# Kernel optimization log

Measured on AMD Instinct MI355X. Metric: run time of the kernel, lower is better.

The kernel has to match this reference:

```python
import jax, jax.numpy as jnp
import numpy as np

HEADS = 16
HEAD_DIM = 64
EMBED = HEADS * HEAD_DIM  # 1024
B, S = 2, 2048


def setup_inputs() -> dict:
    key = jax.random.key(0)
    ks = jax.random.split(key, 9)
    return {
        "value": jax.random.normal(ks[0], (B, S, EMBED), dtype=jnp.float32),
        "key": jax.random.normal(ks[1], (B, S, EMBED), dtype=jnp.float32),
        "query": jax.random.normal(ks[2], (B, S, EMBED), dtype=jnp.float32),
        "mask": jax.random.randint(ks[3], (B, 1, S, S), 0, 2, dtype=jnp.int32),
        "Wq": jax.random.normal(ks[4], (HEAD_DIM, HEAD_DIM), dtype=jnp.float32) * 0.02,
        "Wk": jax.random.normal(ks[5], (HEAD_DIM, HEAD_DIM), dtype=jnp.float32) * 0.02,
        "Wv": jax.random.normal(ks[6], (HEAD_DIM, HEAD_DIM), dtype=jnp.float32) * 0.02,
        "Wo": jax.random.normal(ks[7], (EMBED, EMBED), dtype=jnp.float32) * 0.02,
        "bo": jnp.zeros((EMBED,), dtype=jnp.float32),
    }


def reference(value, key, query, mask, Wq, Wk, Wv, Wo, bo):
    N, Lv = value.shape[0], value.shape[1]
    Lk, Lq = key.shape[1], query.shape[1]
    # Faithful to original: plain reshape (N, heads, len, head_dim), NOT transpose.
    v = value.reshape(N, HEADS, Lv, HEAD_DIM)
    k = key.reshape(N, HEADS, Lk, HEAD_DIM)
    q = query.reshape(N, HEADS, Lq, HEAD_DIM)
    # Per-head Linear (no bias): x @ W.T
    V = jnp.einsum('bhld,ed->bhle', v, Wv)
    K = jnp.einsum('bhld,ed->bhle', k, Wk)
    Q = jnp.einsum('bhld,ed->bhle', q, Wq)
    score = jnp.einsum('bhqd,bhkd->bhqk', Q, K)  # [B,H,Sq,Sk]
    score = jnp.where(mask == 0, jnp.float32(-1e20), score)
    # Faithful quirk: scale by sqrt(embed_size), not sqrt(head_dim)
    scale = jnp.float32(EMBED ** 0.5)
    attn = jax.nn.softmax(score / scale, axis=3)
    out = jnp.einsum('bhqk,bhkd->bhqd', attn, V).reshape(N, Lq, HEADS * HEAD_DIM)
    return out @ Wo.T + bo
```

## Files before the change

### kernel.cpp

```cpp
#include <hip/hip_runtime.h>
#include <hip/hip_bf16.h>
#include <cstdint>
#include <cstddef>

#define S_LEN 2048
#define N_HEADS 16
#define HD 64
#define EMB 1024
#define N_BATCH 2
#define N_BH (N_BATCH * N_HEADS)

typedef __attribute__((ext_vector_type(4))) float f32x4;
typedef __attribute__((ext_vector_type(16))) float f32x16;
typedef __attribute__((ext_vector_type(8))) short short8;
typedef __attribute__((ext_vector_type(8))) _Float16 half8;

__device__ __forceinline__ f32x4 mfma16h(half8 a, half8 b, f32x4 c) {
    return __builtin_amdgcn_mfma_f32_16x16x32_f16(a, b, c, 0, 0, 0);
}
__device__ __forceinline__ f32x16 mfma32h(half8 a, half8 b, f32x16 c) {
    return __builtin_amdgcn_mfma_f32_32x32x16_f16(a, b, c, 0, 0, 0);
}

__device__ __forceinline__ unsigned pkh(float a, float b) {
    return __builtin_bit_cast(unsigned, __builtin_amdgcn_cvt_pkrtz(a, b));
}

#if __has_builtin(__builtin_amdgcn_exp2f)
__device__ __forceinline__ float fast_exp2(float x) { return __builtin_amdgcn_exp2f(x); }
#else
__device__ __forceinline__ float fast_exp2(float x) { return exp2f(x); }
#endif

__global__ __launch_bounds__(256) void prep_kernel(
    const float* __restrict__ q_in, const float* __restrict__ k_in,
    const float* __restrict__ v_in,
    const float* __restrict__ Wq, const float* __restrict__ Wk,
    const float* __restrict__ Wv, const float* __restrict__ Wo,
    const int* __restrict__ mask,
    short* __restrict__ Qb, short* __restrict__ Kb, short* __restrict__ Vt,
    short* __restrict__ Woh, unsigned long long* __restrict__ bits) {
    __shared__ short Al[64 * 72];
    __shared__ short Wl[64 * 72];
    __shared__ short Ol[64 * 72];
    int bx = blockIdx.x;
    int t = threadIdx.x;

    if (bx >= 3072) {
        if (bx < 5120) {
            int gw = (bx - 3072) * 4 + (t >> 6);
            int lane = t & 63;
            const int* src = mask + (size_t)gw * 1024 + lane;
            int row = gw >> 1;
            int bb = row >> 11, qq = row & 2047;
            int wbase = (gw & 1) * 16;
#pragma unroll
            for (int r = 0; r < 16; r++) {
                unsigned long long w = __ballot(src[r * 64] != 0);
                if (lane == 0)
                    bits[((size_t)(bb * 32 + wbase + r) << 11) + qq] = w;
            }
        } else {
            int i = (bx - 5120) * 256 + t;
            f32x4 a = reinterpret_cast<const f32x4*>(Wo)[i * 2];
            f32x4 b = reinterpret_cast<const f32x4*>(Wo)[i * 2 + 1];
            uint4 u = { pkh(a.x, a.y), pkh(a.z, a.w), pkh(b.x, b.y), pkh(b.z, b.w) };
            reinterpret_cast<uint4*>(Woh)[i] = u;
        }
        return;
    }

    int rt = bx & 31;
    int bh = (bx >> 5) & 31;
    int tz = bx >> 10;
    const float* src = (tz == 0 ? q_in : tz == 1 ? k_in : v_in)
                       + (size_t)bh * S_LEN * HD + (size_t)rt * 64 * HD;
    const float* W = (tz == 0 ? Wq : tz == 1 ? Wk : Wv);

#pragma unroll
    for (int r = 0; r < 4; r++) {
        int f4 = t + 256 * r;
        int row = f4 >> 4;
        int c4 = (f4 & 15) * 4;
        f32x4 a = reinterpret_cast<const f32x4*>(src)[f4];
        uint2 ua = { pkh(a.x, a.y), pkh(a.z, a.w) };
        *reinterpret_cast<uint2*>(&Al[row * 72 + c4]) = ua;
        f32x4 w = reinterpret_cast<const f32x4*>(W)[f4];
        uint2 uw = { pkh(w.x, w.y), pkh(w.z, w.w) };
        *reinterpret_cast<uint2*>(&Wl[row * 72 + c4]) = uw;
    }
    __syncthreads();

    int wave = t >> 6, lane = t & 63, quad = lane >> 4, col = lane & 15;
    half8 a0 = *reinterpret_cast<const half8*>(&Al[(wave * 16 + col) * 72 + quad * 8]);
    half8 a1 = *reinterpret_cast<const half8*>(&Al[(wave * 16 + col) * 72 + 32 + quad * 8]);

    const float C1 = 0.04508422002777448f;
    float scl = (tz == 0) ? C1 : 1.0f;

    f32x4 acc[4];
#pragma unroll
    for (int jt = 0; jt < 4; jt++) {
        half8 b0 = *reinterpret_cast<const half8*>(&Wl[(jt * 16 + col) * 72 + quad * 8]);
        half8 b1 = *reinterpret_cast<const half8*>(&Wl[(jt * 16 + col) * 72 + 32 + quad * 8]);
        f32x4 c = {0.f, 0.f, 0.f, 0.f};
        c = mfma16h(a0, b0, c);
        c = mfma16h(a1, b1, c);
        acc[jt] = c;
    }
    __syncthreads();

    if (tz < 2) {
#pragma unroll
        for (int jt = 0; jt < 4; jt++)
#pragma unroll
            for (int i = 0; i < 4; i++)
                Ol[(wave * 16 + quad * 4 + i) * 72 + jt * 16 + col] =
                    __builtin_bit_cast(short, (_Float16)(acc[jt][i] * scl));
        __syncthreads();
        short* dst = (tz == 0 ? Qb : Kb) + (size_t)bh * S_LEN * HD + (size_t)rt * 64 * HD;
        int row = t >> 2, ck = (t & 3) * 16;
        short8 o0 = *reinterpret_cast<const short8*>(&Ol[row * 72 + ck]);
        short8 o1 = *reinterpret_cast<const short8*>(&Ol[row * 72 + ck + 8]);
        *reinterpret_cast<short8*>(&dst[row * 64 + ck]) = o0;
        *reinterpret_cast<short8*>(&dst[row * 64 + ck + 8]) = o1;
    } else {
#pragma unroll
        for (int jt = 0; jt < 4; jt++)
#pragma unroll
            for (int i = 0; i < 4; i++)
                Ol[(jt * 16 + col) * 72 + wave * 16 + quad * 4 + i] =
                    __builtin_bit_cast(short, (_Float16)acc[jt][i]);
        __syncthreads();
        short* dst = Vt + (size_t)bh * HD * S_LEN + rt * 64;
        int d = t >> 2, ck = (t & 3) * 16;
        short8 o0 = *reinterpret_cast<const short8*>(&Ol[d * 72 + ck]);
        short8 o1 = *reinterpret_cast<const short8*>(&Ol[d * 72 + ck + 8]);
        *reinterpret_cast<short8*>(&dst[(size_t)d * S_LEN + ck]) = o0;
        *reinterpret_cast<short8*>(&dst[(size_t)d * S_LEN + ck + 8]) = o1;
    }
}

__global__ __launch_bounds__(512, 4) void attn_kernel(
    const short* __restrict__ Qb, const short* __restrict__ Kb,
    const short* __restrict__ Vt, const unsigned long long* __restrict__ mbits,
    short* __restrict__ Xb) {
    int qt = blockIdx.x;
    int bh = blockIdx.y;
    int b = bh >> 4;
    int t = threadIdx.x, wave = t >> 6, lane = t & 63;
    int g = wave & 3, h = wave >> 2;
    int l5 = lane >> 5, l31 = lane & 31;

    __shared__ short smem[26880];
    short* Pg = smem + 16384 + wave * 1280;

    const short* Qh = Qb + (size_t)bh * S_LEN * HD;
    const short* Kh = Kb + (size_t)bh * S_LEN * HD;
    const short* Vh = Vt + (size_t)bh * HD * S_LEN;
    int qbase = qt * 128 + g * 32;
    int q = qbase + l31;

    half8 qf[4];
#pragma unroll
    for (int kc = 0; kc < 4; kc++)
        qf[kc] = *reinterpret_cast<const half8*>(&Qh[(size_t)q * HD + kc * 16 + l5 * 8]);

    const unsigned long long* mcol = mbits + ((size_t)(b * 32) << 11);
    unsigned long long mwq = mcol[q];

    int r0 = t >> 3, cc = t & 7;
    int dstoff = r0 * 64 + ((cc ^ (r0 & 7)) * 8);
    const short* kg0 = Kh + r0 * HD + cc * 8;
    const short* vg0 = Vh + (size_t)r0 * S_LEN + cc * 8;

    short8 pk = *reinterpret_cast<const short8*>(kg0);
    short8 pv = *reinterpret_cast<const short8*>(vg0);
    *reinterpret_cast<short8*>(&smem[dstoff]) = pk;
    *reinterpret_cast<short8*>(&smem[4096 + dstoff]) = pv;
    __syncthreads();

    f32x16 o0, o1;
#pragma unroll
    for (int r = 0; r < 16; r++) { o0[r] = 0.f; o1[r] = 0.f; }
    float l_acc = 0.f;
    int krow = h * 32 + l31;

    for (int kt = 0; kt < 32; kt++) {
        unsigned long long mwq_n;
        if (kt < 31) {
            pk = *reinterpret_cast<const short8*>(kg0 + (kt + 1) * 4096);
            pv = *reinterpret_cast<const short8*>(vg0 + (kt + 1) * 64);
            mwq_n = mcol[((size_t)(kt + 1) << 11) + q];
        }
        const short* Kbs = smem + (kt & 1) * 8192;
        const short* Vbs = Kbs + 4096;

        f32x16 s;
#pragma unroll
        for (int r = 0; r < 16; r++) s[r] = 0.f;
#pragma unroll
        for (int kc = 0; kc < 4; kc++) {
            half8 ka = *reinterpret_cast<const half8*>(
                &Kbs[krow * 64 + (((kc * 2 + l5) ^ (krow & 7)) * 8)]);
            s = mfma32h(ka, qf[kc], s);
        }
        unsigned gs = (unsigned)(mwq >> (h * 32)) >> (4 * l5);
        float p[16];
#pragma unroll
        for (int r = 0; r < 16; r++) {
            int bitc = (r & 3) + 8 * (r >> 2);
            p[r] = fast_exp2(((gs >> bitc) & 1u) ? s[r] : -200.0f);
            l_acc += p[r];
        }
#pragma unroll
        for (int u = 0; u < 4; u++) {
            uint2 dw = { pkh(p[4 * u], p[4 * u + 1]), pkh(p[4 * u + 2], p[4 * u + 3]) };
            *reinterpret_cast<uint2*>(&Pg[l31 * 40 + 4 * l5 + 8 * u]) = dw;
        }
#pragma unroll
        for (int c = 0; c < 2; c++) {
            half8 pb = *reinterpret_cast<const half8*>(&Pg[l31 * 40 + c * 16 + l5 * 8]);
            {
                int vrow = l31;
                half8 va = *reinterpret_cast<const half8*>(
                    &Vbs[vrow * 64 + (((h * 4 + c * 2 + l5) ^ (vrow & 7)) * 8)]);
                o0 = mfma32h(va, pb, o0);
            }
            {
                int vrow = 32 + l31;
                half8 va = *reinterpret_cast<const half8*>(
                    &Vbs[vrow * 64 + (((h * 4 + c * 2 + l5) ^ (vrow & 7)) * 8)]);
                o1 = mfma32h(va, pb, o1);
            }
        }
        if (kt < 31) {
            short* nb = smem + ((kt + 1) & 1) * 8192;
            *reinterpret_cast<short8*>(&nb[dstoff]) = pk;
            *reinterpret_cast<short8*>(&nb[4096 + dstoff]) = pv;
            mwq = mwq_n;
        }
        __syncthreads();
    }

    l_acc += __shfl_xor(l_acc, 32);
    float* obuf = (float*)smem;
    float* lbuf = (float*)(smem + 26624);
    if (h == 1) {
#pragma unroll
        for (int r = 0; r < 16; r++) {
            obuf[(g * 32 + r) * 64 + lane] = o0[r];
            obuf[(g * 32 + 16 + r) * 64 + lane] = o1[r];
        }
        if (lane < 32) lbuf[g * 32 + lane] = l_acc;
    }
    __syncthreads();
    if (h == 0) {
        float inv = 1.0f / (l_acc + lbuf[g * 32 + l31]);
#pragma unroll
        for (int r = 0; r < 16; r++) {
            o0[r] = (o0[r] + obuf[(g * 32 + r) * 64 + lane]) * inv;
            o1[r] = (o1[r] + obuf[(g * 32 + 16 + r) * 64 + lane]) * inv;
        }
        short* Xrow = Xb + (size_t)bh * S_LEN * HD + (size_t)q * HD;
#pragma unroll
        for (int u = 0; u < 4; u++) {
            uint2 w0 = { pkh(o0[4 * u], o0[4 * u + 1]), pkh(o0[4 * u + 2], o0[4 * u + 3]) };
            *reinterpret_cast<uint2*>(&Xrow[4 * l5 + 8 * u]) = w0;
            uint2 w1 = { pkh(o1[4 * u], o1[4 * u + 1]), pkh(o1[4 * u + 2], o1[4 * u + 3]) };
            *reinterpret_cast<uint2*>(&Xrow[32 + 4 * l5 + 8 * u]) = w1;
        }
    }
}

__global__ __launch_bounds__(512, 4) void final_kernel(
    const short* __restrict__ Xb, const short* __restrict__ Woh,
    const float* __restrict__ bo, float* __restrict__ out) {
    int nb = blockIdx.x;
    int mb = blockIdx.y;
    int t = threadIdx.x, wave = t >> 6, lane = t & 63, quad = lane >> 4, col = lane & 15;
    __shared__ short smem[24576];

    int m0 = mb * 128, n0 = nb * 64;
    int r0 = t >> 3, r1 = r0 + 64, cc = t & 7;
    int dx0 = r0 * 64 + ((cc ^ (r0 & 7)) * 8);
    int dx1 = r1 * 64 + ((cc ^ (r1 & 7)) * 8);
    const short* xg0 = Xb + (size_t)(m0 + r0) * EMB + cc * 8;
    const short* xg1 = Xb + (size_t)(m0 + r1) * EMB + cc * 8;
    const short* wg0 = Woh + (size_t)(n0 + r0) * EMB + cc * 8;

    short8 px0 = *reinterpret_cast<const short8*>(xg0);
    short8 px1 = *reinterpret_cast<const short8*>(xg1);
    short8 pw0 = *reinterpret_cast<const short8*>(wg0);
    *reinterpret_cast<short8*>(&smem[dx0]) = px0;
    *reinterpret_cast<short8*>(&smem[dx1]) = px1;
    *reinterpret_cast<short8*>(&smem[16384 + dx0]) = pw0;
    __syncthreads();

    f32x4 acc[4];
#pragma unroll
    for (int nf = 0; nf < 4; nf++) acc[nf] = (f32x4){0.f, 0.f, 0.f, 0.f};
    int arow = wave * 16 + col;

    for (int s = 0; s < 16; s++) {
        if (s < 15) {
            px0 = *reinterpret_cast<const short8*>(xg0 + (s + 1) * 64);
            px1 = *reinterpret_cast<const short8*>(xg1 + (s + 1) * 64);
            pw0 = *reinterpret_cast<const short8*>(wg0 + (s + 1) * 64);
        }
        const short* Xs = smem + (s & 1) * 8192;
        const short* Ws = smem + 16384 + (s & 1) * 4096;
#pragma unroll
        for (int k2 = 0; k2 < 2; k2++) {
            half8 a = *reinterpret_cast<const half8*>(
                &Xs[arow * 64 + (((k2 * 4 + quad) ^ (arow & 7)) * 8)]);
#pragma unroll
            for (int nf = 0; nf < 4; nf++) {
                int brow = nf * 16 + col;
                half8 bf = *reinterpret_cast<const half8*>(
                    &Ws[brow * 64 + (((k2 * 4 + quad) ^ (brow & 7)) * 8)]);
                acc[nf] = mfma16h(a, bf, acc[nf]);
            }
        }
        if (s < 15) {
            short* Xn = smem + ((s + 1) & 1) * 8192;
            short* Wn = smem + 16384 + ((s + 1) & 1) * 4096;
            *reinterpret_cast<short8*>(&Xn[dx0]) = px0;
            *reinterpret_cast<short8*>(&Xn[dx1]) = px1;
            *reinterpret_cast<short8*>(&Wn[dx0]) = pw0;
        }
        __syncthreads();
    }

#pragma unroll
    for (int nf = 0; nf < 4; nf++) {
        int n = n0 + nf * 16 + col;
        float bb = bo[n];
        int rowb = m0 + wave * 16 + quad * 4;
#pragma unroll
        for (int i = 0; i < 4; i++)
            out[(size_t)(rowb + i) * EMB + n] = acc[nf][i] + bb;
    }
}

extern "C" void kernel_launch(void* const* d_in, const int* in_sizes, int n_in,
                              void* d_out, int out_size, void* d_ws, size_t ws_size,
                              hipStream_t stream) {
    const float* value = (const float*)d_in[0];
    const float* key_  = (const float*)d_in[1];
    const float* query = (const float*)d_in[2];
    const int*   mask  = (const int*)d_in[3];
    const float* Wq = (const float*)d_in[4];
    const float* Wk = (const float*)d_in[5];
    const float* Wv = (const float*)d_in[6];
    const float* Wo = (const float*)d_in[7];
    const float* bo = (const float*)d_in[8];
    float* out = (float*)d_out;

    char* ws = (char*)d_ws;
    short* Qb  = (short*)(ws);
    short* Kb  = (short*)(ws + (size_t)8  * 1048576);
    short* Vt  = (short*)(ws + (size_t)16 * 1048576);
    short* Xb  = (short*)(ws + (size_t)24 * 1048576);
    short* Woh = (short*)(ws + (size_t)32 * 1048576);
    unsigned long long* mbits =
        (unsigned long long*)(ws + (size_t)34 * 1048576);

    prep_kernel<<<dim3(3072 + 2048 + 512), dim3(256), 0, stream>>>(
        query, key_, value, Wq, Wk, Wv, Wo, mask, Qb, Kb, Vt, Woh, mbits);
    attn_kernel<<<dim3(S_LEN / 128, N_BH), dim3(512), 0, stream>>>(Qb, Kb, Vt, mbits, Xb);
    final_kernel<<<dim3(EMB / 64, (N_BATCH * S_LEN) / 128), dim3(512), 0, stream>>>(
        Xb, Woh, bo, out);
}
```

Before: 212.7 us.

## Halve attention block to 64 queries and pass P via lane shuffles

The attention kernel now uses 256-thread blocks covering 64 queries each, so the grid doubles and each thread loads two K/V rows per tile. The probability tile is no longer round-tripped through a per-wave LDS scratch buffer. It is packed to fp16 and exchanged between lane halves with __shfl_xor to build the MFMA B operands directly. This cuts LDS traffic and shared memory per block, which may allow more resident blocks. In exchange, K/V tiles are reused across fewer queries and each block issues more global loads per query.

```diff
diff --git a/kernel.cpp b/kernel.cpp
--- a/kernel.cpp
+++ b/kernel.cpp
@@ -141,7 +141,7 @@
     }
 }
 
-__global__ __launch_bounds__(512, 4) void attn_kernel(
+__global__ __launch_bounds__(256, 4) void attn_kernel(
     const short* __restrict__ Qb, const short* __restrict__ Kb,
     const short* __restrict__ Vt, const unsigned long long* __restrict__ mbits,
     short* __restrict__ Xb) {
@@ -149,16 +149,16 @@
     int bh = blockIdx.y;
     int b = bh >> 4;
     int t = threadIdx.x, wave = t >> 6, lane = t & 63;
-    int g = wave & 3, h = wave >> 2;
+    int g = wave & 1, h = wave >> 1;
     int l5 = lane >> 5, l31 = lane & 31;
 
-    __shared__ short smem[26880];
-    short* Pg = smem + 16384 + wave * 1280;
+    __shared__ short smem[16512];
+    float* lbuf = (float*)(smem + 16384);
 
     const short* Qh = Qb + (size_t)bh * S_LEN * HD;
     const short* Kh = Kb + (size_t)bh * S_LEN * HD;
     const short* Vh = Vt + (size_t)bh * HD * S_LEN;
-    int qbase = qt * 128 + g * 32;
+    int qbase = qt * 64 + g * 32;
     int q = qbase + l31;
 
     half8 qf[4];
@@ -169,15 +169,22 @@
     const unsigned long long* mcol = mbits + ((size_t)(b * 32) << 11);
     unsigned long long mwq = mcol[q];
 
-    int r0 = t >> 3, cc = t & 7;
-    int dstoff = r0 * 64 + ((cc ^ (r0 & 7)) * 8);
+    int r0 = t >> 3, r1 = r0 + 32, cc = t & 7;
+    int dst0 = r0 * 64 + ((cc ^ (r0 & 7)) * 8);
+    int dst1 = r1 * 64 + ((cc ^ (r1 & 7)) * 8);
     const short* kg0 = Kh + r0 * HD + cc * 8;
+    const short* kg1 = Kh + r1 * HD + cc * 8;
     const short* vg0 = Vh + (size_t)r0 * S_LEN + cc * 8;
-
-    short8 pk = *reinterpret_cast<const short8*>(kg0);
-    short8 pv = *reinterpret_cast<const short8*>(vg0);
-    *reinterpret_cast<short8*>(&smem[dstoff]) = pk;
-    *reinterpret_cast<short8*>(&smem[4096 + dstoff]) = pv;
+    const short* vg1 = Vh + (size_t)r1 * S_LEN + cc * 8;
+
+    short8 pk0 = *reinterpret_cast<const short8*>(kg0);
+    short8 pk1 = *reinterpret_cast<const short8*>(kg1);
+    short8 pv0 = *reinterpret_cast<const short8*>(vg0);
+    short8 pv1 = *reinterpret_cast<const short8*>(vg1);
+    *reinterpret_cast<short8*>(&smem[dst0]) = pk0;
+    *reinterpret_cast<short8*>(&smem[dst1]) = pk1;
+    *reinterpret_cast<short8*>(&smem[4096 + dst0]) = pv0;
+    *reinterpret_cast<short8*>(&smem[4096 + dst1]) = pv1;
     __syncthreads();
 
     f32x16 o0, o1;
@@ -189,8 +196,10 @@
     for (int kt = 0; kt < 32; kt++) {
         unsigned long long mwq_n;
         if (kt < 31) {
-            pk = *reinterpret_cast<const short8*>(kg0 + (kt + 1) * 4096);
-            pv = *reinterpret_cast<const short8*>(vg0 + (kt + 1) * 64);
+            pk0 = *reinterpret_cast<const short8*>(kg0 + (kt + 1) * 4096);
+            pk1 = *reinterpret_cast<const short8*>(kg1 + (kt + 1) * 4096);
+            pv0 = *reinterpret_cast<const short8*>(vg0 + (kt + 1) * 64);
+            pv1 = *reinterpret_cast<const short8*>(vg1 + (kt + 1) * 64);
             mwq_n = mcol[((size_t)(kt + 1) << 11) + q];
         }
         const short* Kbs = smem + (kt & 1) * 8192;
@@ -206,38 +215,55 @@
             s = mfma32h(ka, qf[kc], s);
         }
         unsigned gs = (unsigned)(mwq >> (h * 32)) >> (4 * l5);
-        float p[16];
+        float pr[16];
 #pragma unroll
         for (int r = 0; r < 16; r++) {
             int bitc = (r & 3) + 8 * (r >> 2);
-            p[r] = fast_exp2(((gs >> bitc) & 1u) ? s[r] : -200.0f);
-            l_acc += p[r];
-        }
-#pragma unroll
-        for (int u = 0; u < 4; u++) {
-            uint2 dw = { pkh(p[4 * u], p[4 * u + 1]), pkh(p[4 * u + 2], p[4 * u + 3]) };
-            *reinterpret_cast<uint2*>(&Pg[l31 * 40 + 4 * l5 + 8 * u]) = dw;
-        }
-#pragma unroll
-        for (int c = 0; c < 2; c++) {
-            half8 pb = *reinterpret_cast<const half8*>(&Pg[l31 * 40 + c * 16 + l5 * 8]);
-            {
-                int vrow = l31;
-                half8 va = *reinterpret_cast<const half8*>(
-                    &Vbs[vrow * 64 + (((h * 4 + c * 2 + l5) ^ (vrow & 7)) * 8)]);
-                o0 = mfma32h(va, pb, o0);
-            }
-            {
-                int vrow = 32 + l31;
-                half8 va = *reinterpret_cast<const half8*>(
-                    &Vbs[vrow * 64 + (((h * 4 + c * 2 + l5) ^ (vrow & 7)) * 8)]);
-                o1 = mfma32h(va, pb, o1);
-            }
+            pr[r] = fast_exp2(((gs >> bitc) & 1u) ? s[r] : -200.0f);
+            l_acc += pr[r];
+        }
+        unsigned uu[8], xx[8];
+#pragma unroll
+        for (int i = 0; i < 8; i++) uu[i] = pkh(pr[2 * i], pr[2 * i + 1]);
+#pragma unroll
+        for (int i = 0; i < 8; i++)
+            xx[i] = (unsigned)__shfl_xor((int)uu[i], 32);
+        uint4 b0u, b1u;
+        b0u.x = l5 ? xx[2] : uu[0]; b0u.y = l5 ? xx[3] : uu[1];
+        b0u.z = l5 ? uu[2] : xx[0]; b0u.w = l5 ? uu[3] : xx[1];
+        b1u.x = l5 ? xx[6] : uu[4]; b1u.y = l5 ? xx[7] : uu[5];
+        b1u.z = l5 ? uu[6] : xx[4]; b1u.w = l5 ? uu[7] : xx[5];
+        half8 pb0 = __builtin_bit_cast(half8, b0u);
+        half8 pb1 = __builtin_bit_cast(half8, b1u);
+
+        {
+            half8 va = *reinterpret_cast<const half8*>(
+                &Vbs[l31 * 64 + (((h * 4 + l5) ^ (l31 & 7)) * 8)]);
+            o0 = mfma32h(va, pb0, o0);
+        }
+        {
+            int vr = 32 + l31;
+            half8 va = *reinterpret_cast<const half8*>(
+                &Vbs[vr * 64 + (((h * 4 + l5) ^ (vr & 7)) * 8)]);
+            o1 = mfma32h(va, pb0, o1);
+        }
+        {
+            half8 va = *reinterpret_cast<const half8*>(
+                &Vbs[l31 * 64 + (((h * 4 + 2 + l5) ^ (l31 & 7)) * 8)]);
+            o0 = mfma32h(va, pb1, o0);
+        }
+        {
+            int vr = 32 + l31;
+            half8 va = *reinterpret_cast<const half8*>(
+                &Vbs[vr * 64 + (((h * 4 + 2 + l5) ^ (vr & 7)) * 8)]);
+            o1 = mfma32h(va, pb1, o1);
         }
         if (kt < 31) {
             short* nb = smem + ((kt + 1) & 1) * 8192;
-            *reinterpret_cast<short8*>(&nb[dstoff]) = pk;
-            *reinterpret_cast<short8*>(&nb[4096 + dstoff]) = pv;
+            *reinterpret_cast<short8*>(&nb[dst0]) = pk0;
+            *reinterpret_cast<short8*>(&nb[dst1]) = pk1;
+            *reinterpret_cast<short8*>(&nb[4096 + dst0]) = pv0;
+            *reinterpret_cast<short8*>(&nb[4096 + dst1]) = pv1;
             mwq = mwq_n;
         }
         __syncthreads();
@@ -245,7 +271,6 @@
 
     l_acc += __shfl_xor(l_acc, 32);
     float* obuf = (float*)smem;
-    float* lbuf = (float*)(smem + 26624);
     if (h == 1) {
 #pragma unroll
         for (int r = 0; r < 16; r++) {
@@ -368,7 +393,7 @@
 
     prep_kernel<<<dim3(3072 + 2048 + 512), dim3(256), 0, stream>>>(
         query, key_, value, Wq, Wk, Wv, Wo, mask, Qb, Kb, Vt, Woh, mbits);
-    attn_kernel<<<dim3(S_LEN / 128, N_BH), dim3(512), 0, stream>>>(Qb, Kb, Vt, mbits, Xb);
+    attn_kernel<<<dim3(S_LEN / 64, N_BH), dim3(256), 0, stream>>>(Qb, Kb, Vt, mbits, Xb);
     final_kernel<<<dim3(EMB / 64, (N_BATCH * S_LEN) / 128), dim3(512), 0, stream>>>(
         Xb, Woh, bo, out);
 }
```

After: 217.2 us. 1.02x slower.

## Permute K tile rows in LDS so P feeds PV MFMA from registers

Applied to the files above, without the earlier changes.

K rows are stored in LDS in a permuted order, so the S accumulator layout of the QK MFMA already matches the B-operand layout of the PV MFMA. The exp'd probabilities are packed straight into half8 registers. This removes the per-wave P staging buffer and its LDS write/read round trip. LDS use drops, which may allow higher occupancy, but the mask-bit and V-column indexing must exactly match the new permutation.

```diff
diff --git a/kernel.cpp b/kernel.cpp
--- a/kernel.cpp
+++ b/kernel.cpp
@@ -152,8 +152,8 @@
     int g = wave & 3, h = wave >> 2;
     int l5 = lane >> 5, l31 = lane & 31;
 
-    __shared__ short smem[26880];
-    short* Pg = smem + 16384 + wave * 1280;
+    __shared__ short smem[16640];
+    float* lbuf = (float*)(smem + 16384);
 
     const short* Qh = Qb + (size_t)bh * S_LEN * HD;
     const short* Kh = Kb + (size_t)bh * S_LEN * HD;
@@ -170,14 +170,16 @@
     unsigned long long mwq = mcol[q];
 
     int r0 = t >> 3, cc = t & 7;
-    int dstoff = r0 * 64 + ((cc ^ (r0 & 7)) * 8);
+    int kr = (r0 & 32) | ((r0 & 3) + ((r0 & 12) << 1) + ((r0 & 16) >> 2));
+    int dstK = kr * 64 + ((cc ^ (kr & 7)) * 8);
+    int dstV = r0 * 64 + ((cc ^ (r0 & 7)) * 8);
     const short* kg0 = Kh + r0 * HD + cc * 8;
     const short* vg0 = Vh + (size_t)r0 * S_LEN + cc * 8;
 
     short8 pk = *reinterpret_cast<const short8*>(kg0);
     short8 pv = *reinterpret_cast<const short8*>(vg0);
-    *reinterpret_cast<short8*>(&smem[dstoff]) = pk;
-    *reinterpret_cast<short8*>(&smem[4096 + dstoff]) = pv;
+    *reinterpret_cast<short8*>(&smem[dstK]) = pk;
+    *reinterpret_cast<short8*>(&smem[4096 + dstV]) = pv;
     __syncthreads();
 
     f32x16 o0, o1;
@@ -185,6 +187,7 @@
     for (int r = 0; r < 16; r++) { o0[r] = 0.f; o1[r] = 0.f; }
     float l_acc = 0.f;
     int krow = h * 32 + l31;
+    int mshift = h * 32 + 16 * l5;
 
     for (int kt = 0; kt < 32; kt++) {
         unsigned long long mwq_n;
@@ -205,39 +208,39 @@
                 &Kbs[krow * 64 + (((kc * 2 + l5) ^ (krow & 7)) * 8)]);
             s = mfma32h(ka, qf[kc], s);
         }
-        unsigned gs = (unsigned)(mwq >> (h * 32)) >> (4 * l5);
-        float p[16];
-#pragma unroll
-        for (int r = 0; r < 16; r++) {
-            int bitc = (r & 3) + 8 * (r >> 2);
-            p[r] = fast_exp2(((gs >> bitc) & 1u) ? s[r] : -200.0f);
-            l_acc += p[r];
-        }
-#pragma unroll
-        for (int u = 0; u < 4; u++) {
-            uint2 dw = { pkh(p[4 * u], p[4 * u + 1]), pkh(p[4 * u + 2], p[4 * u + 3]) };
-            *reinterpret_cast<uint2*>(&Pg[l31 * 40 + 4 * l5 + 8 * u]) = dw;
-        }
+        unsigned gs2 = (unsigned)(mwq >> mshift);
+        unsigned uu[8];
+#pragma unroll
+        for (int i = 0; i < 8; i++) {
+            float p0 = fast_exp2(((gs2 >> (2 * i)) & 1u) ? s[2 * i] : -200.0f);
+            float p1 = fast_exp2(((gs2 >> (2 * i + 1)) & 1u) ? s[2 * i + 1] : -200.0f);
+            l_acc += p0 + p1;
+            uu[i] = pkh(p0, p1);
+        }
+        uint4 u0 = { uu[0], uu[1], uu[2], uu[3] };
+        uint4 u1 = { uu[4], uu[5], uu[6], uu[7] };
+        half8 pb0 = __builtin_bit_cast(half8, u0);
+        half8 pb1 = __builtin_bit_cast(half8, u1);
+
 #pragma unroll
         for (int c = 0; c < 2; c++) {
-            half8 pb = *reinterpret_cast<const half8*>(&Pg[l31 * 40 + c * 16 + l5 * 8]);
+            half8 pb = c ? pb1 : pb0;
             {
-                int vrow = l31;
-                half8 va = *reinterpret_cast<const half8*>(
-                    &Vbs[vrow * 64 + (((h * 4 + c * 2 + l5) ^ (vrow & 7)) * 8)]);
+                int ch = (h * 4 + l5 * 2 + c) ^ (l31 & 7);
+                half8 va = *reinterpret_cast<const half8*>(&Vbs[l31 * 64 + ch * 8]);
                 o0 = mfma32h(va, pb, o0);
             }
             {
-                int vrow = 32 + l31;
-                half8 va = *reinterpret_cast<const half8*>(
-                    &Vbs[vrow * 64 + (((h * 4 + c * 2 + l5) ^ (vrow & 7)) * 8)]);
+                int vr = 32 + l31;
+                int ch = (h * 4 + l5 * 2 + c) ^ (vr & 7);
+                half8 va = *reinterpret_cast<const half8*>(&Vbs[vr * 64 + ch * 8]);
                 o1 = mfma32h(va, pb, o1);
             }
         }
         if (kt < 31) {
             short* nb = smem + ((kt + 1) & 1) * 8192;
-            *reinterpret_cast<short8*>(&nb[dstoff]) = pk;
-            *reinterpret_cast<short8*>(&nb[4096 + dstoff]) = pv;
+            *reinterpret_cast<short8*>(&nb[dstK]) = pk;
+            *reinterpret_cast<short8*>(&nb[4096 + dstV]) = pv;
             mwq = mwq_n;
         }
         __syncthreads();
@@ -245,7 +248,6 @@
 
     l_acc += __shfl_xor(l_acc, 32);
     float* obuf = (float*)smem;
-    float* lbuf = (float*)(smem + 26624);
     if (h == 1) {
 #pragma unroll
         for (int r = 0; r < 16; r++) {
```

Measured after the change: 207.5 us. 1.02x faster.
